# Kernel tuning notes

Measured on AMD Instinct MI355X. Metric: run time of the kernel, lower is better.

The kernel has to match this reference:

```python
import jax, jax.numpy as jnp
import numpy as np

N_NODES = 50000
N_EDGES = 800000
NUM_RELS = 16
IN_DIM = 16      # == NUM_RELS (one-hot of op_class_id)
H_DIM = 128
OUT_DIM = 128    # must equal H_DIM (actor/critic consume output-layer root feats)
LIN_DIM = 512


def setup_inputs() -> dict:
    key = jax.random.key(0)
    ks = jax.random.split(key, 16)
    op_class_id = jax.random.randint(ks[0], (N_NODES,), 0, NUM_RELS, dtype=jnp.int32)
    norm = jax.random.uniform(ks[1], (N_NODES,), dtype=jnp.float32)
    src = jax.random.randint(ks[2], (N_EDGES,), 0, N_NODES, dtype=jnp.int32)
    dst = jax.random.randint(ks[3], (N_EDGES,), 0, N_NODES, dtype=jnp.int32)
    s = 0.1
    W0 = jax.random.normal(ks[4], (NUM_RELS, IN_DIM, H_DIM), jnp.float32) * s
    W1 = jax.random.normal(ks[5], (NUM_RELS, H_DIM, H_DIM), jnp.float32) * s
    W2 = jax.random.normal(ks[6], (NUM_RELS, H_DIM, OUT_DIM), jnp.float32) * s
    a1_w = jax.random.normal(ks[7], (OUT_DIM, LIN_DIM), jnp.float32) * s
    a1_b = jnp.zeros((LIN_DIM,), jnp.float32)
    a2_w = jax.random.normal(ks[8], (LIN_DIM, OUT_DIM), jnp.float32) * s
    a2_b = jnp.zeros((OUT_DIM,), jnp.float32)
    c1_w = jax.random.normal(ks[9], (OUT_DIM, LIN_DIM), jnp.float32) * s
    c1_b = jnp.zeros((LIN_DIM,), jnp.float32)
    c2_w = jax.random.normal(ks[10], (LIN_DIM, 1), jnp.float32) * s
    c2_b = jnp.zeros((1,), jnp.float32)
    return dict(op_class_id=op_class_id, norm=norm, src=src, dst=dst,
                W0=W0, W1=W1, W2=W2,
                a1_w=a1_w, a1_b=a1_b, a2_w=a2_w, a2_b=a2_b,
                c1_w=c1_w, c1_b=c1_b, c2_w=c2_w, c2_b=c2_b)


def _rgcn_layer(h, cls, norm, src, dst, W, act):
    # per-node relation-specific transform: h[n] @ W[cls[n]]
    # compute all relations then select (R small, avoids [N,in,out] gather)
    stacked = jnp.einsum('ni,rio->rno', h, W)          # [R, N, out]
    msg = stacked[cls, jnp.arange(h.shape[0])]         # [N, out]
    msg = msg * norm[:, None]
    agg = jax.ops.segment_sum(msg[src], dst, num_segments=h.shape[0])
    return act(agg)


def reference(op_class_id, norm, src, dst, W0, W1, W2,
              a1_w, a1_b, a2_w, a2_b, c1_w, c1_b, c2_w, c2_b):
    one_hot = jax.nn.one_hot(op_class_id, IN_DIM, dtype=jnp.float32)  # op_class_one_hot
    h = _rgcn_layer(one_hot, op_class_id, norm, src, dst, W0, jax.nn.relu)
    h = _rgcn_layer(h, op_class_id, norm, src, dst, W1, jax.nn.relu)
    h = _rgcn_layer(h, op_class_id, norm, src, dst, W2,
                    lambda x: jax.nn.softmax(x, axis=1))
    root = h[0]                                        # [OUT_DIM]
    probs = jax.nn.relu(root @ a1_w + a1_b) @ a2_w + a2_b
    value = jax.nn.relu(root @ c1_w + c1_b) @ c2_w + c2_b
    return probs, value
```

## Files before the change

### kernel.cpp

```cpp
#include <hip/hip_runtime.h>

#define NN 50000
#define NE 800000
#define NR 16
#define HD 128
#define LIND 512

#define CAP1 1024
#define CAP0 4096
#define E0CAP 4096
#define E1CAP 32768

#define C_N1 0
#define C_N0 1
#define C_E0 2
#define C_E1 3

#define PZ ((int)0xAAAAAAAA)

__global__ void k_scanA(const int* __restrict__ src, const int* __restrict__ dst,
                        int* map1, int* e0_src, int* cnt) {
    int tid = blockIdx.x * blockDim.x + threadIdx.x;
    int stride = gridDim.x * blockDim.x;
    const int4* d4p = (const int4*)dst;
    for (int q = tid; q < NE / 4; q += stride) {
        int4 d4 = d4p[q];
        int ds[4] = {d4.x, d4.y, d4.z, d4.w};
        #pragma unroll
        for (int j = 0; j < 4; j++) {
            if (ds[j] == 0) {
                int s = src[4 * q + j];
                int i = atomicAdd(&cnt[C_E0], 1) - PZ;
                if (i >= 0 && i < E0CAP) e0_src[i] = s;
                if (atomicCAS(&map1[s], PZ, -2) == PZ) {
                    int slot = atomicAdd(&cnt[C_N1], 1) - PZ;
                    map1[s] = (slot >= 0 && slot < CAP1) ? slot + 2 : 1;
                }
            }
        }
    }
}

__global__ void k_scanB1(const int* __restrict__ src, const int* __restrict__ dst,
                         const int* __restrict__ map1, int* map0,
                         int* e1_src, int* e1_dn, int* cnt) {
    int tid = blockIdx.x * blockDim.x + threadIdx.x;
    int stride = gridDim.x * blockDim.x;
    const int4* d4p = (const int4*)dst;
    for (int q = tid; q < NE / 4; q += stride) {
        int4 d4 = d4p[q];
        int ds[4] = {d4.x, d4.y, d4.z, d4.w};
        #pragma unroll
        for (int j = 0; j < 4; j++) {
            int m = map1[ds[j]];
            if (m >= 2) {
                int s = src[4 * q + j];
                int i = atomicAdd(&cnt[C_E1], 1) - PZ;
                if (i >= 0 && i < E1CAP) { e1_src[i] = s; e1_dn[i] = m - 2; }
                if (atomicCAS(&map0[s], PZ, -2) == PZ) {
                    int slot = atomicAdd(&cnt[C_N0], 1) - PZ;
                    map0[s] = (slot >= 0 && slot < CAP0) ? slot + 2 : 1;
                }
            }
        }
    }
}

__global__ void k_scanB2(const int* __restrict__ src, const int* __restrict__ dst,
                         const int* __restrict__ map0, const int* __restrict__ cls,
                         const float* __restrict__ norm, float* w0sum) {
    int tid = blockIdx.x * blockDim.x + threadIdx.x;
    int stride = gridDim.x * blockDim.x;
    const int4* d4p = (const int4*)dst;
    for (int q = tid; q < NE / 4; q += stride) {
        int4 d4 = d4p[q];
        int ds[4] = {d4.x, d4.y, d4.z, d4.w};
        #pragma unroll
        for (int j = 0; j < 4; j++) {
            int m = map0[ds[j]];
            if (m >= 2) {
                int s = src[4 * q + j];
                atomicAdd(&w0sum[((size_t)(m - 2) << 4) + cls[s]], norm[s]);
            }
        }
    }
}

__global__ void __launch_bounds__(128)
k_edge1(const int* __restrict__ cnt, const int* __restrict__ e1_src,
        const int* __restrict__ e1_dn, const int* __restrict__ map0,
        const int* __restrict__ cls, const float* __restrict__ norm,
        const float* __restrict__ W0, const float* __restrict__ W1,
        const float* __restrict__ w0sum, float* agg1) {
    int t = threadIdx.x;
    int e1n = cnt[C_E1] - PZ;
    if (e1n < 0) e1n = 0; if (e1n > E1CAP) e1n = E1CAP;
    __shared__ float shw[NR];
    __shared__ float sha[HD];
    for (int ei = blockIdx.x; ei < e1n; ei += gridDim.x) {
        int s = e1_src[ei];
        int dn = e1_dn[ei];
        int c = cls[s];
        float nm = norm[s];
        int sslot = map0[s] - 2;
        if (sslot < 0 || sslot >= CAP0) continue;
        if (t < NR) shw[t] = w0sum[((size_t)sslot << 4) + t];
        __syncthreads();
        float a = 0.f;
        #pragma unroll
        for (int cc = 0; cc < NR; cc++) a = fmaf(shw[cc], W0[cc * 2176 + t], a);
        sha[t] = fmaxf(a, 0.f);
        __syncthreads();
        const float* w = W1 + c * (HD * HD) + t;
        float acc = 0.f;
        #pragma unroll 16
        for (int i = 0; i < HD; i++) acc = fmaf(sha[i], w[i << 7], acc);
        atomicAdd(&agg1[((size_t)dn << 7) + t], acc * nm);
        __syncthreads();
    }
}

__global__ void __launch_bounds__(256)
k_root(const int* __restrict__ cnt, const int* __restrict__ e0_src,
       const int* __restrict__ map1, const int* __restrict__ cls,
       const float* __restrict__ norm, const float* __restrict__ agg1,
       const float* __restrict__ W2, float* rootpre) {
    int t = threadIdx.x;
    int c = blockIdx.x;
    __shared__ float u[HD];
    __shared__ int   sl[256];
    __shared__ int   sc[256];
    __shared__ float sn[256];
    __shared__ int any;
    if (t < HD) u[t] = 0.f;
    if (t == 0) any = 0;
    __syncthreads();
    int e0n = cnt[C_E0] - PZ;
    if (e0n < 0) e0n = 0; if (e0n > E0CAP) e0n = E0CAP;

    for (int base = 0; base < e0n; base += 256) {
        int nchunk = e0n - base; if (nchunk > 256) nchunk = 256;
        if (t < nchunk) {
            int s = e0_src[base + t];
            sl[t] = map1[s] - 2;
            sc[t] = cls[s];
            sn[t] = norm[s];
        }
        __syncthreads();
        for (int i = 0; i < nchunk; i++) {
            if (sc[i] != c) continue;
            int slot = sl[i];
            if (slot < 0 || slot >= CAP1) continue;
            if (t < HD) u[t] += sn[i] * fmaxf(agg1[((size_t)slot << 7) + t], 0.f);
            if (t == 0) any = 1;
        }
        __syncthreads();
    }
    if (!any) return;
    int o = t & 127, hf = t >> 7, k0 = hf << 6;
    const float* w2 = W2 + c * (HD * HD);
    float acc = 0.f;
    #pragma unroll 16
    for (int k = k0; k < k0 + 64; k++) acc = fmaf(u[k], w2[(k << 7) + o], acc);
    atomicAdd(&rootpre[o], acc);
}

__global__ void __launch_bounds__(256)
k_mlp(const float* __restrict__ rootpre,
      const float* __restrict__ a1w, const float* __restrict__ a1b,
      const float* __restrict__ a2w, const float* __restrict__ a2b,
      const float* __restrict__ c1w, const float* __restrict__ c1b,
      const float* __restrict__ c2w, const float* __restrict__ c2b,
      float* out) {
    __shared__ float sha[HD];
    __shared__ float shz[64];
    __shared__ float red[256];
    int t = threadIdx.x;
    if (t < HD) sha[t] = rootpre[t];
    __syncthreads();
    float mx = -3.0e38f;
    for (int i = 0; i < HD; i++) mx = fmaxf(mx, sha[i]);
    float ex = (t < HD) ? expf(sha[t] - mx) : 0.f;
    __syncthreads();
    if (t < HD) sha[t] = ex;
    __syncthreads();
    float sum = 0.f;
    for (int i = 0; i < HD; i++) sum += sha[i];
    __syncthreads();
    if (t < HD) sha[t] = ex / sum;
    __syncthreads();

    int m = blockIdx.x >> 3, g = blockIdx.x & 7, k0 = g << 6;
    const float* Wh = m ? c1w : a1w;
    const float* bh = m ? c1b : a1b;
    {
        int o = t & 63, qu = t >> 6, kk0 = qu << 5;
        float z = 0.f;
        #pragma unroll 8
        for (int i = kk0; i < kk0 + 32; i++) z = fmaf(sha[i], Wh[i * LIND + k0 + o], z);
        red[t] = z;
        __syncthreads();
        if (t < 64)
            shz[t] = fmaxf(bh[k0 + t] + red[t] + red[t + 64] + red[t + 128] + red[t + 192], 0.f);
    }
    __syncthreads();
    if (m == 0) {
        int o = t & 127, hf = t >> 7, j0 = hf << 5;
        float acc = 0.f;
        #pragma unroll 8
        for (int j = j0; j < j0 + 32; j++) acc = fmaf(shz[j], a2w[(k0 + j) * HD + o], acc);
        red[t] = acc;
        __syncthreads();
        if (t < HD) {
            float v = red[t] + red[t + 128];
            if (blockIdx.x == 0) v += a2b[t];
            atomicAdd(&out[t], v);
        }
    } else {
        if (t < 64) red[t] = shz[t] * c2w[k0 + t];
        __syncthreads();
        if (t == 0) {
            float v = (blockIdx.x == 8) ? c2b[0] : 0.f;
            for (int j = 0; j < 64; j++) v += red[j];
            atomicAdd(&out[HD], v);
        }
    }
}

extern "C" void kernel_launch(void* const* d_in, const int* in_sizes, int n_in,
                              void* d_out, int out_size, void* d_ws, size_t ws_size,
                              hipStream_t stream) {
    const int*   cls  = (const int*)d_in[0];
    const float* norm = (const float*)d_in[1];
    const int*   src  = (const int*)d_in[2];
    const int*   dst  = (const int*)d_in[3];
    const float* W0   = (const float*)d_in[4];
    const float* W1   = (const float*)d_in[5];
    const float* W2   = (const float*)d_in[6];
    const float* a1w  = (const float*)d_in[7];
    const float* a1b  = (const float*)d_in[8];
    const float* a2w  = (const float*)d_in[9];
    const float* a2b  = (const float*)d_in[10];
    const float* c1w  = (const float*)d_in[11];
    const float* c1b  = (const float*)d_in[12];
    const float* c2w  = (const float*)d_in[13];
    const float* c2b  = (const float*)d_in[14];
    float* out = (float*)d_out;

    char* ws = (char*)d_ws;
    int*   cnt     = (int*)(ws + 0);
    int*   map1    = (int*)(ws + 64);
    int*   map0    = (int*)(ws + 200064);
    int*   e0_src  = (int*)(ws + 400064);
    int*   e1_src  = (int*)(ws + 416448);
    int*   e1_dn   = (int*)(ws + 547520);
    float* rootpre = (float*)(ws + 678592);
    float* w0sum   = (float*)(ws + 679104);
    float* agg1    = (float*)(ws + 941248);

    k_scanA<<<1024, 256, 0, stream>>>(src, dst, map1, e0_src, cnt);
    k_scanB1<<<1024, 256, 0, stream>>>(src, dst, map1, map0, e1_src, e1_dn, cnt);
    k_scanB2<<<1024, 256, 0, stream>>>(src, dst, map0, cls, norm, w0sum);
    k_edge1<<<256, 128, 0, stream>>>(cnt, e1_src, e1_dn, map0, cls, norm, W0, W1, w0sum, agg1);
    k_root<<<NR, 256, 0, stream>>>(cnt, e0_src, map1, cls, norm, agg1, W2, rootpre);
    k_mlp<<<16, 256, 0, stream>>>(rootpre, a1w, a1b, a2w, a2b, c1w, c1b, c2w, c2b, out);
}
```

Before: 137.6 us.

## Fuse edge1, root and MLP kernels into one launch with atomic-counter barriers

Merges the last three kernels into a single launch. Blocks are split by role (edge workers, per-relation root reducers, MLP blocks), and the later stages spin on global done counters with acquire/release atomics. This removes two kernel launch gaps from the tail. It cuts edge-worker blocks from 256 to 128, leaving half of each 256-thread worker block idle. It also relies on all 160 blocks being co-resident to avoid deadlock and on the done counters starting at the workspace poison value.

```diff
diff --git a/kernel.cpp b/kernel.cpp
--- a/kernel.cpp
+++ b/kernel.cpp
@@ -17,6 +17,9 @@
 #define C_E1 3
 
 #define PZ ((int)0xAAAAAAAA)
+
+#define NBE 128
+#define TB_TOTAL (NBE + NR + 16)
 
 __global__ void k_scanA(const int* __restrict__ src, const int* __restrict__ dst,
                         int* map1, int* e0_src, int* cnt) {
@@ -86,143 +89,170 @@
     }
 }
 
-__global__ void __launch_bounds__(128)
-k_edge1(const int* __restrict__ cnt, const int* __restrict__ e1_src,
-        const int* __restrict__ e1_dn, const int* __restrict__ map0,
-        const int* __restrict__ cls, const float* __restrict__ norm,
-        const float* __restrict__ W0, const float* __restrict__ W1,
-        const float* __restrict__ w0sum, float* agg1) {
-    int t = threadIdx.x;
-    int e1n = cnt[C_E1] - PZ;
-    if (e1n < 0) e1n = 0; if (e1n > E1CAP) e1n = E1CAP;
-    __shared__ float shw[NR];
-    __shared__ float sha[HD];
-    for (int ei = blockIdx.x; ei < e1n; ei += gridDim.x) {
-        int s = e1_src[ei];
-        int dn = e1_dn[ei];
-        int c = cls[s];
-        float nm = norm[s];
-        int sslot = map0[s] - 2;
-        if (sslot < 0 || sslot >= CAP0) continue;
-        if (t < NR) shw[t] = w0sum[((size_t)sslot << 4) + t];
-        __syncthreads();
-        float a = 0.f;
-        #pragma unroll
-        for (int cc = 0; cc < NR; cc++) a = fmaf(shw[cc], W0[cc * 2176 + t], a);
-        sha[t] = fmaxf(a, 0.f);
-        __syncthreads();
-        const float* w = W1 + c * (HD * HD) + t;
-        float acc = 0.f;
-        #pragma unroll 16
-        for (int i = 0; i < HD; i++) acc = fmaf(sha[i], w[i << 7], acc);
-        atomicAdd(&agg1[((size_t)dn << 7) + t], acc * nm);
-        __syncthreads();
-    }
-}
-
 __global__ void __launch_bounds__(256)
-k_root(const int* __restrict__ cnt, const int* __restrict__ e0_src,
-       const int* __restrict__ map1, const int* __restrict__ cls,
-       const float* __restrict__ norm, const float* __restrict__ agg1,
-       const float* __restrict__ W2, float* rootpre) {
-    int t = threadIdx.x;
-    int c = blockIdx.x;
-    __shared__ float u[HD];
-    __shared__ int   sl[256];
-    __shared__ int   sc[256];
-    __shared__ float sn[256];
-    __shared__ int any;
-    if (t < HD) u[t] = 0.f;
-    if (t == 0) any = 0;
-    __syncthreads();
-    int e0n = cnt[C_E0] - PZ;
-    if (e0n < 0) e0n = 0; if (e0n > E0CAP) e0n = E0CAP;
-
-    for (int base = 0; base < e0n; base += 256) {
-        int nchunk = e0n - base; if (nchunk > 256) nchunk = 256;
-        if (t < nchunk) {
-            int s = e0_src[base + t];
-            sl[t] = map1[s] - 2;
-            sc[t] = cls[s];
-            sn[t] = norm[s];
-        }
-        __syncthreads();
-        for (int i = 0; i < nchunk; i++) {
-            if (sc[i] != c) continue;
-            int slot = sl[i];
-            if (slot < 0 || slot >= CAP1) continue;
-            if (t < HD) u[t] += sn[i] * fmaxf(agg1[((size_t)slot << 7) + t], 0.f);
-            if (t == 0) any = 1;
-        }
-        __syncthreads();
-    }
-    if (!any) return;
-    int o = t & 127, hf = t >> 7, k0 = hf << 6;
-    const float* w2 = W2 + c * (HD * HD);
-    float acc = 0.f;
-    #pragma unroll 16
-    for (int k = k0; k < k0 + 64; k++) acc = fmaf(u[k], w2[(k << 7) + o], acc);
-    atomicAdd(&rootpre[o], acc);
-}
-
-__global__ void __launch_bounds__(256)
-k_mlp(const float* __restrict__ rootpre,
-      const float* __restrict__ a1w, const float* __restrict__ a1b,
-      const float* __restrict__ a2w, const float* __restrict__ a2b,
-      const float* __restrict__ c1w, const float* __restrict__ c1b,
-      const float* __restrict__ c2w, const float* __restrict__ c2b,
-      float* out) {
-    __shared__ float sha[HD];
-    __shared__ float shz[64];
-    __shared__ float red[256];
-    int t = threadIdx.x;
-    if (t < HD) sha[t] = rootpre[t];
-    __syncthreads();
-    float mx = -3.0e38f;
-    for (int i = 0; i < HD; i++) mx = fmaxf(mx, sha[i]);
-    float ex = (t < HD) ? expf(sha[t] - mx) : 0.f;
-    __syncthreads();
-    if (t < HD) sha[t] = ex;
-    __syncthreads();
-    float sum = 0.f;
-    for (int i = 0; i < HD; i++) sum += sha[i];
-    __syncthreads();
-    if (t < HD) sha[t] = ex / sum;
-    __syncthreads();
-
-    int m = blockIdx.x >> 3, g = blockIdx.x & 7, k0 = g << 6;
-    const float* Wh = m ? c1w : a1w;
-    const float* bh = m ? c1b : a1b;
-    {
-        int o = t & 63, qu = t >> 6, kk0 = qu << 5;
-        float z = 0.f;
-        #pragma unroll 8
-        for (int i = kk0; i < kk0 + 32; i++) z = fmaf(sha[i], Wh[i * LIND + k0 + o], z);
-        red[t] = z;
-        __syncthreads();
-        if (t < 64)
-            shz[t] = fmaxf(bh[k0 + t] + red[t] + red[t + 64] + red[t + 128] + red[t + 192], 0.f);
-    }
-    __syncthreads();
-    if (m == 0) {
-        int o = t & 127, hf = t >> 7, j0 = hf << 5;
-        float acc = 0.f;
-        #pragma unroll 8
-        for (int j = j0; j < j0 + 32; j++) acc = fmaf(shz[j], a2w[(k0 + j) * HD + o], acc);
-        red[t] = acc;
-        __syncthreads();
-        if (t < HD) {
-            float v = red[t] + red[t + 128];
-            if (blockIdx.x == 0) v += a2b[t];
-            atomicAdd(&out[t], v);
+k_tail(const int* __restrict__ cnt, const int* __restrict__ e1_src,
+       const int* __restrict__ e1_dn, const int* __restrict__ map0,
+       const int* __restrict__ e0_src, const int* __restrict__ map1,
+       const int* __restrict__ cls, const float* __restrict__ norm,
+       const float* __restrict__ W0, const float* __restrict__ W1,
+       const float* __restrict__ W2, const float* __restrict__ w0sum,
+       float* agg1, float* rootpre, int* done,
+       const float* __restrict__ a1w, const float* __restrict__ a1b,
+       const float* __restrict__ a2w, const float* __restrict__ a2b,
+       const float* __restrict__ c1w, const float* __restrict__ c1b,
+       const float* __restrict__ c2w, const float* __restrict__ c2b,
+       float* out) {
+    const int t = threadIdx.x;
+    const int b = blockIdx.x;
+
+    if (b < NBE) {
+        __shared__ float shw[NR];
+        __shared__ float sha[HD];
+        int e1n = cnt[C_E1] - PZ;
+        if (e1n < 0) e1n = 0; if (e1n > E1CAP) e1n = E1CAP;
+        for (int ei = b; ei < e1n; ei += NBE) {
+            int s = e1_src[ei];
+            int dn = e1_dn[ei];
+            int c = cls[s];
+            float nm = norm[s];
+            int sslot = map0[s] - 2;
+            if (sslot < 0 || sslot >= CAP0) continue;
+            if (t < NR) shw[t] = w0sum[((size_t)sslot << 4) + t];
+            __syncthreads();
+            if (t < HD) {
+                float a = 0.f;
+                #pragma unroll
+                for (int cc = 0; cc < NR; cc++) a = fmaf(shw[cc], W0[cc * 2176 + t], a);
+                sha[t] = fmaxf(a, 0.f);
+            }
+            __syncthreads();
+            if (t < HD) {
+                const float* w = W1 + c * (HD * HD) + t;
+                float acc = 0.f;
+                #pragma unroll 16
+                for (int i = 0; i < HD; i++) acc = fmaf(sha[i], w[i << 7], acc);
+                atomicAdd(&agg1[((size_t)dn << 7) + t], acc * nm);
+            }
+            __syncthreads();
+        }
+        __syncthreads();
+        if (t == 0) {
+            __threadfence();
+            __hip_atomic_fetch_add(&done[0], 1, __ATOMIC_RELEASE, __HIP_MEMORY_SCOPE_AGENT);
+        }
+    } else if (b < NBE + NR) {
+        const int c = b - NBE;
+        __shared__ float u[HD];
+        __shared__ int   sl[256];
+        __shared__ int   sc[256];
+        __shared__ float sn[256];
+        __shared__ int any;
+        if (t < HD) u[t] = 0.f;
+        if (t == 0) {
+            any = 0;
+            while (__hip_atomic_load(&done[0], __ATOMIC_ACQUIRE,
+                                     __HIP_MEMORY_SCOPE_AGENT) - PZ < NBE)
+                __builtin_amdgcn_s_sleep(8);
+        }
+        __syncthreads();
+        int e0n = cnt[C_E0] - PZ;
+        if (e0n < 0) e0n = 0; if (e0n > E0CAP) e0n = E0CAP;
+        for (int base = 0; base < e0n; base += 256) {
+            int nchunk = e0n - base; if (nchunk > 256) nchunk = 256;
+            if (t < nchunk) {
+                int s = e0_src[base + t];
+                sl[t] = map1[s] - 2;
+                sc[t] = cls[s];
+                sn[t] = norm[s];
+            }
+            __syncthreads();
+            for (int i = 0; i < nchunk; i++) {
+                if (sc[i] != c) continue;
+                int slot = sl[i];
+                if (slot < 0 || slot >= CAP1) continue;
+                if (t < HD) {
+                    float v = __hip_atomic_load(&agg1[((size_t)slot << 7) + t],
+                                                __ATOMIC_RELAXED, __HIP_MEMORY_SCOPE_AGENT);
+                    u[t] += sn[i] * fmaxf(v, 0.f);
+                }
+                if (t == 0) any = 1;
+            }
+            __syncthreads();
+        }
+        if (any) {
+            int o = t & 127, hf = t >> 7, k0 = hf << 6;
+            const float* w2 = W2 + c * (HD * HD);
+            float acc = 0.f;
+            #pragma unroll 16
+            for (int k = k0; k < k0 + 64; k++) acc = fmaf(u[k], w2[(k << 7) + o], acc);
+            atomicAdd(&rootpre[o], acc);
+        }
+        __syncthreads();
+        if (t == 0) {
+            __threadfence();
+            __hip_atomic_fetch_add(&done[1], 1, __ATOMIC_RELEASE, __HIP_MEMORY_SCOPE_AGENT);
         }
     } else {
-        if (t < 64) red[t] = shz[t] * c2w[k0 + t];
-        __syncthreads();
-        if (t == 0) {
-            float v = (blockIdx.x == 8) ? c2b[0] : 0.f;
-            for (int j = 0; j < 64; j++) v += red[j];
-            atomicAdd(&out[HD], v);
+        const int bb = b - NBE - NR;
+        __shared__ float sha[HD];
+        __shared__ float shz[64];
+        __shared__ float red[256];
+        if (t == 0) {
+            while (__hip_atomic_load(&done[1], __ATOMIC_ACQUIRE,
+                                     __HIP_MEMORY_SCOPE_AGENT) - PZ < NR)
+                __builtin_amdgcn_s_sleep(8);
+        }
+        __syncthreads();
+        if (t < HD)
+            sha[t] = __hip_atomic_load(&rootpre[t], __ATOMIC_RELAXED,
+                                       __HIP_MEMORY_SCOPE_AGENT);
+        __syncthreads();
+        float mx = -3.0e38f;
+        for (int i = 0; i < HD; i++) mx = fmaxf(mx, sha[i]);
+        float ex = (t < HD) ? expf(sha[t] - mx) : 0.f;
+        __syncthreads();
+        if (t < HD) sha[t] = ex;
+        __syncthreads();
+        float sum = 0.f;
+        for (int i = 0; i < HD; i++) sum += sha[i];
+        __syncthreads();
+        if (t < HD) sha[t] = ex / sum;
+        __syncthreads();
+
+        int m = bb >> 3, g = bb & 7, k0 = g << 6;
+        const float* Wh = m ? c1w : a1w;
+        const float* bh = m ? c1b : a1b;
+        {
+            int o = t & 63, qu = t >> 6, kk0 = qu << 5;
+            float z = 0.f;
+            #pragma unroll 8
+            for (int i = kk0; i < kk0 + 32; i++) z = fmaf(sha[i], Wh[i * LIND + k0 + o], z);
+            red[t] = z;
+            __syncthreads();
+            if (t < 64)
+                shz[t] = fmaxf(bh[k0 + t] + red[t] + red[t + 64] + red[t + 128] + red[t + 192], 0.f);
+        }
+        __syncthreads();
+        if (m == 0) {
+            int o = t & 127, hf = t >> 7, j0 = hf << 5;
+            float acc = 0.f;
+            #pragma unroll 8
+            for (int j = j0; j < j0 + 32; j++) acc = fmaf(shz[j], a2w[(k0 + j) * HD + o], acc);
+            red[t] = acc;
+            __syncthreads();
+            if (t < HD) {
+                float v = red[t] + red[t + 128];
+                if (bb == 0) v += a2b[t];
+                atomicAdd(&out[t], v);
+            }
+        } else {
+            if (t < 64) red[t] = shz[t] * c2w[k0 + t];
+            __syncthreads();
+            if (t == 0) {
+                float v = (bb == 8) ? c2b[0] : 0.f;
+                for (int j = 0; j < 64; j++) v += red[j];
+                atomicAdd(&out[HD], v);
+            }
         }
     }
 }
@@ -257,11 +287,13 @@
     float* rootpre = (float*)(ws + 678592);
     float* w0sum   = (float*)(ws + 679104);
     float* agg1    = (float*)(ws + 941248);
+    int*   done    = (int*)(ws + 1500032);
 
     k_scanA<<<1024, 256, 0, stream>>>(src, dst, map1, e0_src, cnt);
     k_scanB1<<<1024, 256, 0, stream>>>(src, dst, map1, map0, e1_src, e1_dn, cnt);
     k_scanB2<<<1024, 256, 0, stream>>>(src, dst, map0, cls, norm, w0sum);
-    k_edge1<<<256, 128, 0, stream>>>(cnt, e1_src, e1_dn, map0, cls, norm, W0, W1, w0sum, agg1);
-    k_root<<<NR, 256, 0, stream>>>(cnt, e0_src, map1, cls, norm, agg1, W2, rootpre);
-    k_mlp<<<16, 256, 0, stream>>>(rootpre, a1w, a1b, a2w, a2b, c1w, c1b, c2w, c2b, out);
-}
+    k_tail<<<TB_TOTAL, 256, 0, stream>>>(cnt, e1_src, e1_dn, map0, e0_src, map1,
+                                         cls, norm, W0, W1, W2, w0sum,
+                                         agg1, rootpre, done,
+                                         a1w, a1b, a2w, a2b, c1w, c1b, c2w, c2b, out);
+}
```

Measured after the change: 147.9 us. +7.6%, slower.
